# Optimization experiments

Hardware: AMD Instinct MI355X
Metric: run time of the kernel (lower is better)

## Reference

```python
import jax, jax.numpy as jnp
import numpy as np


def setup_inputs() -> dict:
    key = jax.random.key(0)
    k1, k2, k3, k4, k5 = jax.random.split(key, 5)
    B, C, H, W = 8, 512, 64, 64
    mid = C // 8
    x = jax.random.normal(k1, (B, C, H, W), dtype=jnp.float32)
    # 1x1 convs (no bias) are just channel-mixing matrices
    Wb = jax.random.normal(k2, (mid, C), dtype=jnp.float32) * (1.0 / np.sqrt(C))
    Wc = jax.random.normal(k3, (mid, C), dtype=jnp.float32) * (1.0 / np.sqrt(C))
    Wd = jax.random.normal(k4, (C, C), dtype=jnp.float32) * (1.0 / np.sqrt(C))
    gamma = jax.random.normal(k5, (1,), dtype=jnp.float32)
    return {"x": x, "Wb": Wb, "Wc": Wc, "Wd": Wd, "gamma": gamma}


def reference(x, Wb, Wc, Wd, gamma):
    B, C, H, W = x.shape
    N = H * W
    xf = x.reshape(B, C, N)                          # (B, C, N)
    b = jnp.einsum('mc,bcn->bnm', Wb, xf)            # queries  (B, N, mid)
    c = jnp.einsum('mc,bcn->bmn', Wc, xf)            # keys     (B, mid, N)
    d = jnp.einsum('oc,bcn->bno', Wd, xf)            # values   (B, N, C)
    # unscaled scores, softmax over keys (last dim), as in the source
    attn = jax.nn.softmax(jnp.einsum('bnm,bmk->bnk', b, c), axis=-1)  # (B, N, N)
    out = jnp.einsum('bnk,bko->bno', attn, d)        # (B, N, C)
    out = out.transpose(0, 2, 1).reshape(B, C, H, W)
    return gamma * out + x
```

## Files before the change

kernel.cpp:

```cpp
#include <hip/hip_runtime.h>

typedef unsigned short u16;
typedef _Float16 f16x8 __attribute__((ext_vector_type(8)));
typedef short bf16x8 __attribute__((ext_vector_type(8)));
typedef float f32x16 __attribute__((ext_vector_type(16)));
typedef unsigned int u32x4 __attribute__((ext_vector_type(4)));

#define LOG2E 1.44269504088896340736f

static __device__ __forceinline__ u16 f2h(float f){
  union { _Float16 h; u16 u; } v; v.h = (_Float16)f; return v.u;
}
static __device__ __forceinline__ u16 f2bf(float f){
  union { float f; unsigned u; } v; v.f = f;
  return (u16)((v.u + 0x7fffu + ((v.u >> 16) & 1u)) >> 16);
}
static __device__ __forceinline__ unsigned pk2bf(float lo, float hi){
  unsigned r; asm("v_cvt_pk_bf16_f32 %0, %1, %2" : "=v"(r) : "v"(lo), "v"(hi)); return r;
}
static __device__ __forceinline__ float ex2(float x){
#if __has_builtin(__builtin_amdgcn_exp2f)
  return __builtin_amdgcn_exp2f(x);
#else
  return exp2f(x);
#endif
}
#define PSWAP(a, b) asm("v_permlane32_swap_b32 %0, %1" : "+v"(a), "+v"(b))

__global__ __launch_bounds__(256) void k_tr(const float* __restrict__ x, u16* __restrict__ xt){
  int bx = blockIdx.x;
  int nb = bx & 63, cb = (bx >> 6) & 7, b = bx >> 9;
  __shared__ u16 lt[64 * 68];
  int t = threadIdx.x;
  int cl = t >> 4, n0 = (t & 15) * 4;
  const float* xp = x + ((size_t)(b * 512 + cb * 64)) * 4096 + nb * 64;
#pragma unroll
  for (int i = 0; i < 4; ++i) {
    int c = cl + i * 16;
    float4 v = *(const float4*)(xp + (size_t)c * 4096 + n0);
    u16* d = &lt[c * 68 + n0];
    d[0] = f2h(v.x); d[1] = f2h(v.y); d[2] = f2h(v.z); d[3] = f2h(v.w);
  }
  __syncthreads();
  u16* xo = xt + ((size_t)(b * 4096 + nb * 64)) * 512 + cb * 64;
#pragma unroll
  for (int i = 0; i < 2; ++i) {
    int s = t + i * 256;
    int n = s >> 3, ch = s & 7;
    u32x4 o;
#pragma unroll
    for (int j = 0; j < 4; ++j) {
      u16 a = lt[(ch * 8 + 2 * j) * 68 + n];
      u16 bb = lt[(ch * 8 + 2 * j + 1) * 68 + n];
      o[j] = (unsigned)a | ((unsigned)bb << 16);
    }
    *(u32x4*)(xo + (size_t)n * 512 + ch * 8) = o;
  }
}

__global__ __launch_bounds__(512) void k_pqk(const u16* __restrict__ xt, const float* __restrict__ wb,
                                             const float* __restrict__ wc, u16* __restrict__ qk){
  int bx = blockIdx.x;
  int nb = bx & 31, b = bx >> 5;
  __shared__ u16 lx[128 * 64];
  __shared__ u16 lw[128 * 64];
  int t = threadIdx.x, w = t >> 6, l = t & 63, hi = l >> 5, ln = l & 31;
  int wr = w >> 1, wcol = w & 1;
  f32x16 acc[2] = {};
  for (int kt = 0; kt < 8; ++kt) {
    int c0 = kt * 64;
#pragma unroll
    for (int i = 0; i < 2; ++i) {
      int s = t + i * 512; int row = s >> 3, ch = s & 7;
      u32x4 v = *(const u32x4*)(xt + ((size_t)(b * 4096 + nb * 128 + row)) * 512 + c0 + ch * 8);
      *(u32x4*)((char*)lx + ((row * 128 + ch * 16) ^ ((row & 7) << 4))) = v;
    }
#pragma unroll
    for (int i = 0; i < 4; ++i) {
      int s = t + i * 512; int row = s >> 4, c4 = s & 15;
      const float* src = (row < 64) ? (wb + (size_t)row * 512 + c0 + c4 * 4)
                                    : (wc + (size_t)(row - 64) * 512 + c0 + c4 * 4);
      float4 v = *(const float4*)src;
      float sc = (row < 64) ? LOG2E : 1.0f;
      unsigned lo = (unsigned)f2h(v.x * sc) | ((unsigned)f2h(v.y * sc) << 16);
      unsigned h2 = (unsigned)f2h(v.z * sc) | ((unsigned)f2h(v.w * sc) << 16);
      unsigned long long qv = ((unsigned long long)h2 << 32) | lo;
      *(unsigned long long*)((char*)lw + ((row * 128 + c4 * 8) ^ ((row & 7) << 4))) = qv;
    }
    __syncthreads();
#pragma unroll
    for (int cc = 0; cc < 4; ++cc) {
      int ra = wr * 32 + ln;
      f16x8 a = *(const f16x8*)((char*)lx + ((ra * 128 + cc * 32 + hi * 16) ^ ((ra & 7) << 4)));
#pragma unroll
      for (int mt = 0; mt < 2; ++mt) {
        int rb = wcol * 64 + mt * 32 + ln;
        f16x8 bb = *(const f16x8*)((char*)lw + ((rb * 128 + cc * 32 + hi * 16) ^ ((rb & 7) << 4)));
        acc[mt] = __builtin_amdgcn_mfma_f32_32x32x16_f16(a, bb, acc[mt], 0, 0, 0);
      }
    }
    __syncthreads();
  }
#pragma unroll
  for (int mt = 0; mt < 2; ++mt)
#pragma unroll
    for (int r = 0; r < 16; ++r) {
      int n = wr * 32 + (r & 3) + 8 * (r >> 2) + 4 * hi;
      int m = wcol * 64 + mt * 32 + ln;
      qk[((size_t)(b * 4096 + nb * 128 + n)) * 128 + m] = f2h(acc[mt][r]);
    }
}

template <int OBF>
__global__ __launch_bounds__(512) void k_pv(const u16* __restrict__ xt, const float* __restrict__ wd,
                                            u16* __restrict__ vt){
  int bx = blockIdx.x;
  int nb = bx & 31, ob = (bx >> 5) & 3, b = bx >> 7;
  __shared__ u16 lx[128 * 64];
  __shared__ u16 lw[128 * 64];
  int t = threadIdx.x, w = t >> 6, l = t & 63, hi = l >> 5, ln = l & 31;
  int wr = w >> 2, wn = w & 3;
  f32x16 acc[2] = {};
  for (int kt = 0; kt < 8; ++kt) {
    int c0 = kt * 64;
#pragma unroll
    for (int i = 0; i < 2; ++i) {
      int s = t + i * 512; int row = s >> 3, ch = s & 7;
      u32x4 v = *(const u32x4*)(xt + ((size_t)(b * 4096 + nb * 128 + row)) * 512 + c0 + ch * 8);
      *(u32x4*)((char*)lx + ((row * 128 + ch * 16) ^ ((row & 7) << 4))) = v;
    }
#pragma unroll
    for (int i = 0; i < 4; ++i) {
      int s = t + i * 512; int row = s >> 4, c4 = s & 15;
      const float* src = wd + (size_t)(ob * 128 + row) * 512 + c0 + c4 * 4;
      float4 v = *(const float4*)src;
      unsigned lo = (unsigned)f2h(v.x) | ((unsigned)f2h(v.y) << 16);
      unsigned h2 = (unsigned)f2h(v.z) | ((unsigned)f2h(v.w) << 16);
      unsigned long long qv = ((unsigned long long)h2 << 32) | lo;
      *(unsigned long long*)((char*)lw + ((row * 128 + c4 * 8) ^ ((row & 7) << 4))) = qv;
    }
    __syncthreads();
#pragma unroll
    for (int cc = 0; cc < 4; ++cc) {
      int rb = wn * 32 + ln;
      f16x8 bb = *(const f16x8*)((char*)lx + ((rb * 128 + cc * 32 + hi * 16) ^ ((rb & 7) << 4)));
#pragma unroll
      for (int ot = 0; ot < 2; ++ot) {
        int ra = wr * 64 + ot * 32 + ln;
        f16x8 a = *(const f16x8*)((char*)lw + ((ra * 128 + cc * 32 + hi * 16) ^ ((ra & 7) << 4)));
        acc[ot] = __builtin_amdgcn_mfma_f32_32x32x16_f16(a, bb, acc[ot], 0, 0, 0);
      }
    }
    __syncthreads();
  }
#pragma unroll
  for (int ot = 0; ot < 2; ++ot)
#pragma unroll
    for (int r = 0; r < 16; ++r) {
      int o = ob * 128 + wr * 64 + ot * 32 + (r & 3) + 8 * (r >> 2) + 4 * hi;
      int n = nb * 128 + wn * 32 + ln;
      vt[((size_t)(b * 512 + o)) * 4096 + n] = OBF ? f2bf(acc[ot][r]) : f2h(acc[ot][r]);
    }
}

__global__ __launch_bounds__(512, 1) void k_attn2(const u16* __restrict__ qk, const u16* __restrict__ vt,
                                                  const float* __restrict__ x, const float* __restrict__ gamma,
                                                  float* __restrict__ out){
  __shared__ char smem[40960];
  int bx = blockIdx.x;
  int orig = (bx & 7) * 32 + (bx >> 3);
  int combo = orig >> 4, qt = orig & 15;
  int b = combo >> 1, oc2 = combo & 1;
  int obase = oc2 * 256;
  int t = threadIdx.x, w = t >> 6, l = t & 63, hi = l >> 5, ln = l & 31;
  int q = qt * 256 + w * 32 + ln;
  size_t b4096 = (size_t)b * 4096;
  f16x8 qf[4];
  {
    const u16* qrow = qk + (b4096 + q) * 128;
#pragma unroll
    for (int ch = 0; ch < 4; ++ch) qf[ch] = *(const f16x8*)(qrow + ch * 16 + hi * 8);
  }
  int rowS = t >> 3, chS = t & 7;
  unsigned wOff = (unsigned)(rowS * 128 + ((chS * 16) ^ ((rowS & 7) << 4)));
  unsigned rb[4];
#pragma unroll
  for (int cc = 0; cc < 4; ++cc)
    rb[cc] = (unsigned)(ln * 128 + (((cc << 5) | (hi << 4)) ^ ((ln & 7) << 4)));
  const u16* gK = qk + (b4096 + rowS) * 128 + 64 + chS * 8;
  const u16* gV0 = vt + ((size_t)(b * 512 + obase + rowS)) * 4096 + chS * 8;
  const u16* gV1 = gV0 + (size_t)64 * 4096;
  const u16* gV2 = gV0 + (size_t)128 * 4096;
  const u16* gV3 = gV0 + (size_t)192 * 4096;
  u32x4 kreg = *(const u32x4*)gK;
  u32x4 vr0 = *(const u32x4*)gV0, vr1 = *(const u32x4*)gV1;
  u32x4 vr2 = *(const u32x4*)gV2, vr3 = *(const u32x4*)gV3;
  f32x16 acc[8] = {};
  float lacc = 0.0f;
  for (int kt = 0; kt < 64; ++kt) {
    *(u32x4*)(smem + wOff)         = kreg;
    *(u32x4*)(smem + 8192  + wOff) = vr0;
    *(u32x4*)(smem + 16384 + wOff) = vr1;
    *(u32x4*)(smem + 24576 + wOff) = vr2;
    *(u32x4*)(smem + 32768 + wOff) = vr3;
    __syncthreads();
    if (kt < 63) {
      gK += 8192; gV0 += 64; gV1 += 64; gV2 += 64; gV3 += 64;
      kreg = *(const u32x4*)gK;
      vr0 = *(const u32x4*)gV0; vr1 = *(const u32x4*)gV1;
      vr2 = *(const u32x4*)gV2; vr3 = *(const u32x4*)gV3;
    }
    f32x16 s0 = {}, s1 = {};
    __builtin_amdgcn_s_setprio(1);
#pragma unroll
    for (int cc = 0; cc < 4; ++cc) {
      f16x8 k0 = *(const f16x8*)(smem + rb[cc]);
      f16x8 k1 = *(const f16x8*)(smem + 4096 + rb[cc]);
      s0 = __builtin_amdgcn_mfma_f32_32x32x16_f16(k0, qf[cc], s0, 0, 0, 0);
      s1 = __builtin_amdgcn_mfma_f32_32x32x16_f16(k1, qf[cc], s1, 0, 0, 0);
    }
    __builtin_amdgcn_s_setprio(0);
#pragma unroll
    for (int r = 0; r < 16; ++r) s0[r] = ex2(s0[r]);
#pragma unroll
    for (int r = 0; r < 16; ++r) s1[r] = ex2(s1[r]);
    {
      float p[16];
#pragma unroll
      for (int r = 0; r < 16; ++r) p[r] = s0[r] + s1[r];
#pragma unroll
      for (int d = 8; d >= 1; d >>= 1)
#pragma unroll
        for (int r = 0; r < d; ++r) p[r] += p[r + d];
      lacc += p[0];
    }
    unsigned c0[8], c1[8];
#pragma unroll
    for (int i = 0; i < 8; ++i) c0[i] = pk2bf(s0[2 * i], s0[2 * i + 1]);
#pragma unroll
    for (int i = 0; i < 8; ++i) c1[i] = pk2bf(s1[2 * i], s1[2 * i + 1]);
    PSWAP(c0[0], c0[2]); PSWAP(c0[1], c0[3]); PSWAP(c0[4], c0[6]); PSWAP(c0[5], c0[7]);
    PSWAP(c1[0], c1[2]); PSWAP(c1[1], c1[3]); PSWAP(c1[4], c1[6]); PSWAP(c1[5], c1[7]);
    union U8 { unsigned u[4]; bf16x8 v; } pa[4];
#pragma unroll
    for (int j = 0; j < 4; ++j) { pa[0].u[j] = c0[j]; pa[1].u[j] = c0[4 + j]; pa[2].u[j] = c1[j]; pa[3].u[j] = c1[4 + j]; }
    __builtin_amdgcn_s_setprio(1);
#pragma unroll
    for (int kc = 0; kc < 4; ++kc) {
#pragma unroll
      for (int ot = 0; ot < 8; ++ot) {
        bf16x8 vb = *(const bf16x8*)(smem + 8192 + ot * 4096 + rb[kc]);
        acc[ot] = __builtin_amdgcn_mfma_f32_32x32x16_bf16(pa[kc].v, vb, acc[ot], 0, 0, 0);
      }
    }
    __builtin_amdgcn_s_setprio(0);
    __syncthreads();
  }
  float l_tot = lacc + __shfl_xor(lacc, 32);
  float sinv = gamma[0] / l_tot;
  __syncthreads();
  float* tb = (float*)smem + w * 1056;
#pragma unroll
  for (int ot = 0; ot < 8; ++ot) {
#pragma unroll
    for (int r = 0; r < 16; ++r) {
      int qr = (r & 3) + 8 * (r >> 2) + 4 * hi;
      tb[ln * 33 + qr] = acc[ot][r];
    }
#pragma unroll
    for (int it = 0; it < 16; ++it) {
      int orow = it * 2 + hi;
      float v = tb[orow * 33 + ln];
      size_t gi = (((size_t)(b * 512 + obase + ot * 32 + orow)) << 12) + (size_t)(qt * 256 + w * 32 + ln);
      out[gi] = sinv * v + x[gi];
    }
  }
}

extern "C" void kernel_launch(void* const* d_in, const int* in_sizes, int n_in,
                              void* d_out, int out_size, void* d_ws, size_t ws_size,
                              hipStream_t stream) {
  (void)in_sizes; (void)n_in; (void)out_size; (void)ws_size;
  const float* x     = (const float*)d_in[0];
  const float* wb    = (const float*)d_in[1];
  const float* wc    = (const float*)d_in[2];
  const float* wd    = (const float*)d_in[3];
  const float* gamma = (const float*)d_in[4];
  float* out = (float*)d_out;
  char* ws = (char*)d_ws;
  u16* xt  = (u16*)ws;
  u16* qkb = (u16*)(ws + 33554432);
  u16* vtb = (u16*)(ws + 41943040);
  k_tr   <<<dim3(4096), dim3(256), 0, stream>>>(x, xt);
  k_pqk  <<<dim3(256),  dim3(512), 0, stream>>>(xt, wb, wc, qkb);
  k_pv<1><<<dim3(1024), dim3(512), 0, stream>>>(xt, wd, vtb);
  k_attn2<<<dim3(256),  dim3(512), 0, stream>>>(qkb, vtb, x, gamma, out);
}
```

Baseline: 252.7 us.

## Rework attention kernel with double-buffered direct-to-LDS loads and 2 query tiles per wave

The attention kernel moves from 512-thread blocks with register-staged K/V loads to 256-thread blocks (two per CU). K/V tiles are fetched with global_load_lds straight into a double-buffered LDS area, which removes the register round trip and one barrier per iteration. Each wave now handles 64 queries against 128 output channels instead of 32 queries against 256. That reuses each V fragment across two query tiles and doubles the grid to 512 blocks. The risks are higher register pressure and correctness of the swizzled LDS layout used by the direct loads.

```diff
diff --git a/kernel.cpp b/kernel.cpp
--- a/kernel.cpp
+++ b/kernel.cpp
@@ -26,6 +26,10 @@
 #endif
 }
 #define PSWAP(a, b) asm("v_permlane32_swap_b32 %0, %1" : "+v"(a), "+v"(b))
+
+typedef __attribute__((address_space(3))) unsigned int lds_u32;
+typedef __attribute__((address_space(1))) const unsigned int glob_u32;
+#define GLL(gp, lp) __builtin_amdgcn_global_load_lds((glob_u32*)(gp), (lds_u32*)(lp), 16, 0, 0)
 
 __global__ __launch_bounds__(256) void k_tr(const float* __restrict__ x, u16* __restrict__ xt){
   int bx = blockIdx.x;
@@ -111,7 +115,6 @@
     }
 }
 
-template <int OBF>
 __global__ __launch_bounds__(512) void k_pv(const u16* __restrict__ xt, const float* __restrict__ wd,
                                             u16* __restrict__ vt){
   int bx = blockIdx.x;
@@ -159,120 +162,165 @@
     for (int r = 0; r < 16; ++r) {
       int o = ob * 128 + wr * 64 + ot * 32 + (r & 3) + 8 * (r >> 2) + 4 * hi;
       int n = nb * 128 + wn * 32 + ln;
-      vt[((size_t)(b * 512 + o)) * 4096 + n] = OBF ? f2bf(acc[ot][r]) : f2h(acc[ot][r]);
-    }
-}
-
-__global__ __launch_bounds__(512, 1) void k_attn2(const u16* __restrict__ qk, const u16* __restrict__ vt,
+      vt[((size_t)(b * 512 + o)) * 4096 + n] = f2bf(acc[ot][r]);
+    }
+}
+
+__global__ __launch_bounds__(256, 2) void k_attn3(const u16* __restrict__ qk, const u16* __restrict__ vt,
                                                   const float* __restrict__ x, const float* __restrict__ gamma,
                                                   float* __restrict__ out){
-  __shared__ char smem[40960];
+  __shared__ char smem[49152];
   int bx = blockIdx.x;
-  int orig = (bx & 7) * 32 + (bx >> 3);
+  int orig = (bx & 7) * 64 + (bx >> 3);
   int combo = orig >> 4, qt = orig & 15;
-  int b = combo >> 1, oc2 = combo & 1;
-  int obase = oc2 * 256;
+  int b = combo >> 2, oc = combo & 3;
+  int obase = oc * 128;
   int t = threadIdx.x, w = t >> 6, l = t & 63, hi = l >> 5, ln = l & 31;
-  int q = qt * 256 + w * 32 + ln;
   size_t b4096 = (size_t)b * 4096;
-  f16x8 qf[4];
+  f16x8 qf0[4], qf1[4];
   {
-    const u16* qrow = qk + (b4096 + q) * 128;
-#pragma unroll
-    for (int ch = 0; ch < 4; ++ch) qf[ch] = *(const f16x8*)(qrow + ch * 16 + hi * 8);
-  }
-  int rowS = t >> 3, chS = t & 7;
-  unsigned wOff = (unsigned)(rowS * 128 + ((chS * 16) ^ ((rowS & 7) << 4)));
-  unsigned rb[4];
+    const u16* q0 = qk + (b4096 + qt * 256 + w * 64 + ln) * 128;
+    const u16* q1 = q0 + 32 * 128;
+#pragma unroll
+    for (int ch = 0; ch < 4; ++ch) {
+      qf0[ch] = *(const f16x8*)(q0 + ch * 16 + hi * 8);
+      qf1[ch] = *(const f16x8*)(q1 + ch * 16 + hi * 8);
+    }
+  }
+  unsigned rbK[4];
 #pragma unroll
   for (int cc = 0; cc < 4; ++cc)
-    rb[cc] = (unsigned)(ln * 128 + (((cc << 5) | (hi << 4)) ^ ((ln & 7) << 4)));
-  const u16* gK = qk + (b4096 + rowS) * 128 + 64 + chS * 8;
-  const u16* gV0 = vt + ((size_t)(b * 512 + obase + rowS)) * 4096 + chS * 8;
-  const u16* gV1 = gV0 + (size_t)64 * 4096;
-  const u16* gV2 = gV0 + (size_t)128 * 4096;
-  const u16* gV3 = gV0 + (size_t)192 * 4096;
-  u32x4 kreg = *(const u32x4*)gK;
-  u32x4 vr0 = *(const u32x4*)gV0, vr1 = *(const u32x4*)gV1;
-  u32x4 vr2 = *(const u32x4*)gV2, vr3 = *(const u32x4*)gV3;
-  f32x16 acc[8] = {};
-  float lacc = 0.0f;
+    rbK[cc] = (unsigned)(ln * 128 + (((cc << 5) | (hi << 4)) ^ ((ln & 7) << 4)));
+  int row = t >> 3;
+  int ch2 = ((t & 7) ^ (row & 7)) * 8;
+  const u16* pK = qk + (b4096 + row) * 128 + 64 + ch2;
+  const u16* pV = vt + ((size_t)(b * 512 + obase + row)) * 4096 + ch2;
+  unsigned ldsW = (unsigned)(w * 1024 + (l & 63) * 0);
+  {
+    char* nb = smem;
+    GLL(pK,                 nb + ldsW);
+    GLL(pK + 4096,          nb + 4096 + ldsW);
+    GLL(pV,                 nb + 8192 + ldsW);
+    GLL(pV + 131072,        nb + 12288 + ldsW);
+    GLL(pV + 262144,        nb + 16384 + ldsW);
+    GLL(pV + 393216,        nb + 20480 + ldsW);
+    pK += 8192; pV += 64;
+  }
+  f32x16 acc0[4] = {}, acc1[4] = {};
+  float lacc0 = 0.0f, lacc1 = 0.0f;
   for (int kt = 0; kt < 64; ++kt) {
-    *(u32x4*)(smem + wOff)         = kreg;
-    *(u32x4*)(smem + 8192  + wOff) = vr0;
-    *(u32x4*)(smem + 16384 + wOff) = vr1;
-    *(u32x4*)(smem + 24576 + wOff) = vr2;
-    *(u32x4*)(smem + 32768 + wOff) = vr3;
-    __syncthreads();
+    __syncthreads();
+    char* bufp = smem + (kt & 1) * 24576;
     if (kt < 63) {
-      gK += 8192; gV0 += 64; gV1 += 64; gV2 += 64; gV3 += 64;
-      kreg = *(const u32x4*)gK;
-      vr0 = *(const u32x4*)gV0; vr1 = *(const u32x4*)gV1;
-      vr2 = *(const u32x4*)gV2; vr3 = *(const u32x4*)gV3;
-    }
-    f32x16 s0 = {}, s1 = {};
+      char* nb = smem + ((kt + 1) & 1) * 24576;
+      GLL(pK,                 nb + ldsW);
+      GLL(pK + 4096,          nb + 4096 + ldsW);
+      GLL(pV,                 nb + 8192 + ldsW);
+      GLL(pV + 131072,        nb + 12288 + ldsW);
+      GLL(pV + 262144,        nb + 16384 + ldsW);
+      GLL(pV + 393216,        nb + 20480 + ldsW);
+      pK += 8192; pV += 64;
+    }
+    f32x16 s00 = {}, s01 = {}, s10 = {}, s11 = {};
     __builtin_amdgcn_s_setprio(1);
 #pragma unroll
     for (int cc = 0; cc < 4; ++cc) {
-      f16x8 k0 = *(const f16x8*)(smem + rb[cc]);
-      f16x8 k1 = *(const f16x8*)(smem + 4096 + rb[cc]);
-      s0 = __builtin_amdgcn_mfma_f32_32x32x16_f16(k0, qf[cc], s0, 0, 0, 0);
-      s1 = __builtin_amdgcn_mfma_f32_32x32x16_f16(k1, qf[cc], s1, 0, 0, 0);
+      f16x8 k0 = *(const f16x8*)(bufp + rbK[cc]);
+      f16x8 k1 = *(const f16x8*)(bufp + 4096 + rbK[cc]);
+      s00 = __builtin_amdgcn_mfma_f32_32x32x16_f16(k0, qf0[cc], s00, 0, 0, 0);
+      s01 = __builtin_amdgcn_mfma_f32_32x32x16_f16(k1, qf0[cc], s01, 0, 0, 0);
+      s10 = __builtin_amdgcn_mfma_f32_32x32x16_f16(k0, qf1[cc], s10, 0, 0, 0);
+      s11 = __builtin_amdgcn_mfma_f32_32x32x16_f16(k1, qf1[cc], s11, 0, 0, 0);
     }
     __builtin_amdgcn_s_setprio(0);
-#pragma unroll
-    for (int r = 0; r < 16; ++r) s0[r] = ex2(s0[r]);
-#pragma unroll
-    for (int r = 0; r < 16; ++r) s1[r] = ex2(s1[r]);
+    union U8 { unsigned u[4]; bf16x8 v; } pa0[4], pa1[4];
+#pragma unroll
+    for (int r = 0; r < 16; ++r) s00[r] = ex2(s00[r]);
+#pragma unroll
+    for (int r = 0; r < 16; ++r) s01[r] = ex2(s01[r]);
     {
       float p[16];
 #pragma unroll
-      for (int r = 0; r < 16; ++r) p[r] = s0[r] + s1[r];
+      for (int r = 0; r < 16; ++r) p[r] = s00[r] + s01[r];
 #pragma unroll
       for (int d = 8; d >= 1; d >>= 1)
 #pragma unroll
         for (int r = 0; r < d; ++r) p[r] += p[r + d];
-      lacc += p[0];
-    }
-    unsigned c0[8], c1[8];
-#pragma unroll
-    for (int i = 0; i < 8; ++i) c0[i] = pk2bf(s0[2 * i], s0[2 * i + 1]);
-#pragma unroll
-    for (int i = 0; i < 8; ++i) c1[i] = pk2bf(s1[2 * i], s1[2 * i + 1]);
-    PSWAP(c0[0], c0[2]); PSWAP(c0[1], c0[3]); PSWAP(c0[4], c0[6]); PSWAP(c0[5], c0[7]);
-    PSWAP(c1[0], c1[2]); PSWAP(c1[1], c1[3]); PSWAP(c1[4], c1[6]); PSWAP(c1[5], c1[7]);
-    union U8 { unsigned u[4]; bf16x8 v; } pa[4];
-#pragma unroll
-    for (int j = 0; j < 4; ++j) { pa[0].u[j] = c0[j]; pa[1].u[j] = c0[4 + j]; pa[2].u[j] = c1[j]; pa[3].u[j] = c1[4 + j]; }
+      lacc0 += p[0];
+    }
+    {
+      unsigned c0[8], c1[8];
+#pragma unroll
+      for (int i = 0; i < 8; ++i) c0[i] = pk2bf(s00[2 * i], s00[2 * i + 1]);
+#pragma unroll
+      for (int i = 0; i < 8; ++i) c1[i] = pk2bf(s01[2 * i], s01[2 * i + 1]);
+      PSWAP(c0[0], c0[2]); PSWAP(c0[1], c0[3]); PSWAP(c0[4], c0[6]); PSWAP(c0[5], c0[7]);
+      PSWAP(c1[0], c1[2]); PSWAP(c1[1], c1[3]); PSWAP(c1[4], c1[6]); PSWAP(c1[5], c1[7]);
+#pragma unroll
+      for (int j = 0; j < 4; ++j) { pa0[0].u[j] = c0[j]; pa0[1].u[j] = c0[4 + j]; pa0[2].u[j] = c1[j]; pa0[3].u[j] = c1[4 + j]; }
+    }
+#pragma unroll
+    for (int r = 0; r < 16; ++r) s10[r] = ex2(s10[r]);
+#pragma unroll
+    for (int r = 0; r < 16; ++r) s11[r] = ex2(s11[r]);
+    {
+      float p[16];
+#pragma unroll
+      for (int r = 0; r < 16; ++r) p[r] = s10[r] + s11[r];
+#pragma unroll
+      for (int d = 8; d >= 1; d >>= 1)
+#pragma unroll
+        for (int r = 0; r < d; ++r) p[r] += p[r + d];
+      lacc1 += p[0];
+    }
+    {
+      unsigned c0[8], c1[8];
+#pragma unroll
+      for (int i = 0; i < 8; ++i) c0[i] = pk2bf(s10[2 * i], s10[2 * i + 1]);
+#pragma unroll
+      for (int i = 0; i < 8; ++i) c1[i] = pk2bf(s11[2 * i], s11[2 * i + 1]);
+      PSWAP(c0[0], c0[2]); PSWAP(c0[1], c0[3]); PSWAP(c0[4], c0[6]); PSWAP(c0[5], c0[7]);
+      PSWAP(c1[0], c1[2]); PSWAP(c1[1], c1[3]); PSWAP(c1[4], c1[6]); PSWAP(c1[5], c1[7]);
+#pragma unroll
+      for (int j = 0; j < 4; ++j) { pa1[0].u[j] = c0[j]; pa1[1].u[j] = c0[4 + j]; pa1[2].u[j] = c1[j]; pa1[3].u[j] = c1[4 + j]; }
+    }
     __builtin_amdgcn_s_setprio(1);
 #pragma unroll
     for (int kc = 0; kc < 4; ++kc) {
 #pragma unroll
-      for (int ot = 0; ot < 8; ++ot) {
-        bf16x8 vb = *(const bf16x8*)(smem + 8192 + ot * 4096 + rb[kc]);
-        acc[ot] = __builtin_amdgcn_mfma_f32_32x32x16_bf16(pa[kc].v, vb, acc[ot], 0, 0, 0);
+      for (int ot = 0; ot < 4; ++ot) {
+        bf16x8 vb = *(const bf16x8*)(bufp + 8192 + ot * 4096 + rbK[kc]);
+        acc0[ot] = __builtin_amdgcn_mfma_f32_32x32x16_bf16(pa0[kc].v, vb, acc0[ot], 0, 0, 0);
+        acc1[ot] = __builtin_amdgcn_mfma_f32_32x32x16_bf16(pa1[kc].v, vb, acc1[ot], 0, 0, 0);
       }
     }
     __builtin_amdgcn_s_setprio(0);
-    __syncthreads();
-  }
-  float l_tot = lacc + __shfl_xor(lacc, 32);
-  float sinv = gamma[0] / l_tot;
+  }
+  float g = gamma[0];
+  float l0 = lacc0 + __shfl_xor(lacc0, 32);
+  float l1 = lacc1 + __shfl_xor(lacc1, 32);
+  float sinv0 = g / l0, sinv1 = g / l1;
   __syncthreads();
   float* tb = (float*)smem + w * 1056;
 #pragma unroll
-  for (int ot = 0; ot < 8; ++ot) {
-#pragma unroll
-    for (int r = 0; r < 16; ++r) {
-      int qr = (r & 3) + 8 * (r >> 2) + 4 * hi;
-      tb[ln * 33 + qr] = acc[ot][r];
-    }
-#pragma unroll
-    for (int it = 0; it < 16; ++it) {
-      int orow = it * 2 + hi;
-      float v = tb[orow * 33 + ln];
-      size_t gi = (((size_t)(b * 512 + obase + ot * 32 + orow)) << 12) + (size_t)(qt * 256 + w * 32 + ln);
-      out[gi] = sinv * v + x[gi];
+  for (int qs = 0; qs < 2; ++qs) {
+    float sv = qs ? sinv1 : sinv0;
+    size_t qcol = (size_t)(qt * 256 + w * 64 + qs * 32 + ln);
+#pragma unroll
+    for (int ot = 0; ot < 4; ++ot) {
+      f32x16& av = qs ? acc1[ot] : acc0[ot];
+#pragma unroll
+      for (int r = 0; r < 16; ++r) {
+        int qr = (r & 3) + 8 * (r >> 2) + 4 * hi;
+        tb[ln * 33 + qr] = av[r];
+      }
+#pragma unroll
+      for (int it = 0; it < 16; ++it) {
+        int orow = it * 2 + hi;
+        float v = tb[orow * 33 + ln];
+        size_t gi = (((size_t)(b * 512 + obase + ot * 32 + orow)) << 12) + qcol;
+        out[gi] = sv * v + x[gi];
+      }
     }
   }
 }
@@ -293,6 +341,6 @@
   u16* vtb = (u16*)(ws + 41943040);
   k_tr   <<<dim3(4096), dim3(256), 0, stream>>>(x, xt);
   k_pqk  <<<dim3(256),  dim3(512), 0, stream>>>(xt, wb, wc, qkb);
-  k_pv<1><<<dim3(1024), dim3(512), 0, stream>>>(xt, wd, vtb);
-  k_attn2<<<dim3(256),  dim3(512), 0, stream>>>(qkb, vtb, x, gamma, out);
-}
+  k_pv   <<<dim3(1024), dim3(512), 0, stream>>>(xt, wd, vtb);
+  k_attn3<<<dim3(512),  dim3(256), 0, stream>>>(qkb, vtb, x, gamma, out);
+}
```

Result: slower. 422.1 us (+67.0%).
